# Performance work log

Measured on AMD Instinct MI355X. Metric: run time of the kernel, lower is better.

The kernel has to match this reference:

```python
import jax, jax.numpy as jnp
import numpy as np

B, N, C, H, L, M, V, NC = 8, 2048, 512, 8, 8, 128, 32000, 2
HD = C // H          # head dim = 64
HID = 4 * C          # MLP hidden = 2048
SCALE = HD ** -0.5
LN_EPS = 1e-5
FEAT_EPS = 1e-6


def _orth_matrix(d, m, rng):
    # gaussian_orthogonal_random_matrix: stack QR blocks of d x d
    blocks = []
    n_full, m_rem = divmod(m, d)
    for _ in range(n_full):
        Q, _ = np.linalg.qr(rng.standard_normal((d, d)))
        blocks.append(Q)
    if m_rem > 0:
        Q, _ = np.linalg.qr(rng.standard_normal((d, d)))
        blocks.append(Q[:, :m_rem])
    return np.concatenate(blocks, axis=1)


def setup_inputs() -> dict:
    key = jax.random.key(0)
    ks = jax.random.split(key, 32)
    rng = np.random.default_rng(0)

    def w(i, shape, s=0.02):
        return jax.random.normal(ks[i], shape, jnp.float32) * s

    proj = jnp.asarray(
        np.stack([np.stack([_orth_matrix(HD, M, rng) for _ in range(H)]) for _ in range(L)]),
        jnp.float32)  # [L, H, HD, M]

    inp = {
        "input_ids": jax.random.randint(ks[0], (B, N), 0, V),
        "attention_mask": jnp.ones((B, N), jnp.int32),
        "tok_emb": w(1, (V, C)),
        "cls": w(2, (1, 1, C)),
        "pos": w(3, (N + 1, C)),
        "ln1_g": jnp.ones((L, C), jnp.float32),
        "ln1_b": jnp.zeros((L, C), jnp.float32),
        "qW": w(4, (L, C, C)), "qb": jnp.zeros((L, C), jnp.float32),
        "kW": w(5, (L, C, C)), "kb": jnp.zeros((L, C), jnp.float32),
        "vW": w(6, (L, C, C)), "vb": jnp.zeros((L, C), jnp.float32),
        "oW": w(7, (L, C, C)), "ob": jnp.zeros((L, C), jnp.float32),
        "proj": proj,
        "ln2_g": jnp.ones((L, C), jnp.float32),
        "ln2_b": jnp.zeros((L, C), jnp.float32),
        "fc1W": w(8, (L, C, HID)), "fc1b": jnp.zeros((L, HID), jnp.float32),
        "fc2W": w(9, (L, HID, C)), "fc2b": jnp.zeros((L, C), jnp.float32),
        "lnf_g": jnp.ones((C,), jnp.float32),
        "lnf_b": jnp.zeros((C,), jnp.float32),
        "headW": w(10, (C, NC)),
        "headb": jnp.zeros((NC,), jnp.float32),
    }
    return inp


def _ln(x, g, b):
    mu = jnp.mean(x, axis=-1, keepdims=True)
    var = jnp.mean((x - mu) ** 2, axis=-1, keepdims=True)
    return (x - mu) * jax.lax.rsqrt(var + LN_EPS) * g + b


def _softmax_feature(x, p):
    # x: [B,Nt,H,HD], p: [H,HD,M]
    xw = jnp.einsum('bnhd,hdm->bnhm', x, p)
    x_sq = 0.5 * jnp.sum(x * x, axis=-1, keepdims=True)
    mx = jnp.max(xw, axis=-1, keepdims=True)
    return jnp.exp(xw - mx) * jnp.exp(mx - x_sq) + FEAT_EPS


def reference(input_ids, attention_mask, tok_emb, cls, pos, ln1_g, ln1_b,
              qW, qb, kW, kb, vW, vb, oW, ob, proj, ln2_g, ln2_b,
              fc1W, fc1b, fc2W, fc2b, lnf_g, lnf_b, headW, headb):
    x = tok_emb[input_ids]                                   # [B,N,C]
    x = jnp.concatenate([jnp.broadcast_to(cls, (B, 1, C)), x], axis=1)  # [B,Nt,C]
    x = x + pos[None]
    mask = jnp.concatenate(
        [jnp.ones((B, 1), x.dtype), attention_mask.astype(x.dtype)], axis=1)  # [B,Nt]
    mfeat = mask[:, :, None, None]

    Nt = N + 1
    for i in range(L):
        # Performer attention (FAVOR+)
        y = _ln(x, ln1_g[i], ln1_b[i])
        q = (y @ qW[i] + qb[i]).reshape(B, Nt, H, HD) * SCALE
        k = (y @ kW[i] + kb[i]).reshape(B, Nt, H, HD) * mfeat
        v = (y @ vW[i] + vb[i]).reshape(B, Nt, H, HD) * mfeat
        qf = _softmax_feature(q, proj[i])                    # [B,Nt,H,M]
        kf = _softmax_feature(k, proj[i])
        kv = jnp.einsum('bnhm,bnhd->bhmd', kf, v)            # [B,H,M,HD]
        ksum = jnp.sum(kf, axis=1)                           # [B,H,M]
        denom = jnp.maximum(jnp.einsum('bnhm,bhm->bhn', qf, ksum), 1e-6)[..., None]
        ctx = jnp.einsum('bnhm,bhmd->bhnd', qf, kv) / denom  # [B,H,Nt,HD]
        out = ctx.transpose(0, 2, 1, 3).reshape(B, Nt, C)
        x = x + (out @ oW[i] + ob[i])
        # MLP (exact GELU, as nn.GELU default)
        y = _ln(x, ln2_g[i], ln2_b[i])
        h = jax.nn.gelu(y @ fc1W[i] + fc1b[i], approximate=False)
        x = x + (h @ fc2W[i] + fc2b[i])

    x = _ln(x, lnf_g, lnf_b)
    return x[:, 0] @ headW + headb                           # [B,NC]
```

## Files before the change

### kernel.cpp

```cpp
#include <hip/hip_runtime.h>
#include <cmath>
#include <cstdint>
#include <cstddef>

#define B_ 8
#define N_ 2048
#define NT 2049
#define NP 2080
#define C_ 512
#define H_ 8
#define HD_ 64
#define L_ 8
#define M_ 128
#define HID_ 2048
#define NC_ 2
#define BNT (B_*NT)
#define RP (B_*NP)
#define SCALE_ 0.125f
#define LN_EPS_ 1e-5f
#define FEAT_EPS_ 1e-6f

#define MODE_GELU  2
#define MODE_RESID 3

typedef unsigned short u16;
typedef unsigned short u16x8 __attribute__((ext_vector_type(8)));
typedef short frag __attribute__((ext_vector_type(8)));
typedef float f32x4 __attribute__((ext_vector_type(4)));

constexpr size_t F_X    = 0;
constexpr size_t F_KVP  = F_X   + (size_t)RP*512;
constexpr size_t F_KSP  = F_KVP + (size_t)4*64*8192;
constexpr size_t F_KV   = F_KSP + (size_t)4*64*128;
constexpr size_t F_KS   = F_KV  + (size_t)64*M_*HD_;
constexpr size_t F_QKVB = F_KS  + (size_t)64*M_;
constexpr size_t F_END  = F_QKVB + 1536;
constexpr size_t S_BASE = 2 * F_END;
constexpr size_t S_Y    = S_BASE;
constexpr size_t S_V    = S_Y  + (size_t)RP*512;
constexpr size_t S_KF   = S_V  + (size_t)RP*512;
constexpr size_t S_QF   = S_KF + (size_t)RP*1024;
constexpr size_t S_WQKV = S_QF + (size_t)RP*1024;
constexpr size_t S_WO   = S_WQKV + (size_t)1536*512;
constexpr size_t S_WF1  = S_WO   + (size_t)512*512;
constexpr size_t S_WF2  = S_WF1  + (size_t)2048*512;
constexpr size_t S_PT   = S_WF2  + (size_t)512*2048;
constexpr size_t S_END  = S_PT   + (size_t)8*128*64;
constexpr size_t WS_BYTES = S_END * 2;

__device__ __forceinline__ float wave_reduce(float v) {
#pragma unroll
  for (int off = 32; off > 0; off >>= 1) v += __shfl_down(v, off, 64);
  return v;
}
__device__ __forceinline__ float b2f(u16 u) {
  union { float f; uint32_t i; } v; v.i = ((uint32_t)u) << 16; return v.f;
}
__device__ __forceinline__ u16 f2b(float f) {
  union { float f; uint32_t i; } v; v.f = f;
  uint32_t r = v.i + 0x7FFF + ((v.i >> 16) & 1);
  return (u16)(r >> 16);
}
__device__ __forceinline__ void gstage(const u16* g, u16* lds_base, int lane) {
#if __has_builtin(__builtin_amdgcn_global_load_lds)
  __builtin_amdgcn_global_load_lds((const __attribute__((address_space(1))) void*)g,
      (__attribute__((address_space(3))) void*)lds_base, 16, 0, 0);
#else
  *(u16x8*)(lds_base + lane * 8) = *(const u16x8*)g;
#endif
}

__global__ __launch_bounds__(256) void embed_k(const int* __restrict__ ids,
    const float* __restrict__ tok, const float* __restrict__ cls,
    const float* __restrict__ pos, float* __restrict__ X) {
  int row = blockIdx.x;
  int b = row / NT, n = row - b * NT;
  int t = threadIdx.x;
  const float* src = (n == 0) ? cls : tok + (size_t)ids[b * N_ + n - 1] * C_;
  size_t rp = (size_t)b * NP + n;
  X[rp * C_ + t]       = src[t]       + pos[(size_t)n * C_ + t];
  X[rp * C_ + t + 256] = src[t + 256] + pos[(size_t)n * C_ + t + 256];
}

__global__ __launch_bounds__(256) void wconv_k(
    const float* __restrict__ qW, const float* __restrict__ kW,
    const float* __restrict__ vW, const float* __restrict__ oW,
    const float* __restrict__ f1W, const float* __restrict__ f2W,
    const float* __restrict__ projL,
    const float* __restrict__ qb, const float* __restrict__ kb,
    const float* __restrict__ vb,
    u16* __restrict__ Wqkv, u16* __restrict__ Wo,
    u16* __restrict__ Wf1, u16* __restrict__ Wf2,
    u16* __restrict__ PT, float* __restrict__ QKVB) {
  __shared__ float tile[32][33];
  int bid = blockIdx.x, t = threadIdx.x;
  if (bid >= 3104) {
    int i = (bid - 3104) * 256 + t;
    QKVB[i] = (i < 512) ? qb[i] : (i < 1024) ? kb[i - 512] : vb[i - 1024];
    return;
  }
  if (bid >= 3072) {
    int base = (bid - 3072) * 2048 + t * 8;
#pragma unroll
    for (int j = 0; j < 8; ++j) {
      int idx = base + j;
      int h = idx >> 13, rem = idx & 8191, m = rem >> 6, d = rem & 63;
      PT[idx] = f2b(projL[(size_t)h * 8192 + d * 128 + m]);
    }
    return;
  }
  int ti = t >> 5, tj = t & 31;
  const float* src; u16* dst; int k0, n0, ldn, ldk, scol;
  if (bid < 768) {
    int tk = bid & 15, tn = bid >> 4;
    k0 = tk * 32; n0 = tn * 32;
    int sel = n0 >> 9; scol = n0 & 511;
    src = (sel == 0) ? qW : (sel == 1) ? kW : vW;
    ldn = 512; dst = Wqkv; ldk = 512;
  } else if (bid < 1024) {
    int b2 = bid - 768;
    int tk = b2 & 15, tn = b2 >> 4;
    k0 = tk * 32; n0 = tn * 32; scol = n0;
    src = oW; ldn = 512; dst = Wo; ldk = 512;
  } else if (bid < 2048) {
    int b2 = bid - 1024;
    int tk = b2 & 15, tn = b2 >> 4;
    k0 = tk * 32; n0 = tn * 32; scol = n0;
    src = f1W; ldn = 2048; dst = Wf1; ldk = 512;
  } else {
    int b2 = bid - 2048;
    int tk = b2 & 63, tn = b2 >> 6;
    k0 = tk * 32; n0 = tn * 32; scol = n0;
    src = f2W; ldn = 512; dst = Wf2; ldk = 2048;
  }
  const float* sp = src + (size_t)k0 * ldn + scol;
  u16* dp = dst + (size_t)n0 * ldk + k0;
#pragma unroll
  for (int p = 0; p < 4; ++p)
    tile[ti + p * 8][tj] = sp[(size_t)(ti + p * 8) * ldn + tj];
  __syncthreads();
#pragma unroll
  for (int p = 0; p < 4; ++p)
    dp[(size_t)(ti + p * 8) * ldk + tj] = f2b(tile[tj][ti + p * 8]);
}

__global__ __launch_bounds__(256) void ln_bf_k(const float* __restrict__ X,
    const float* __restrict__ g, const float* __restrict__ b,
    u16* __restrict__ Y) {
  int w = threadIdx.x >> 6, lane = threadIdx.x & 63;
  int row = blockIdx.x * 4 + w;
  const float* xr = X + (size_t)row * C_;
  float v[8];
  *(float4*)&v[0] = *(const float4*)(xr + lane * 8);
  *(float4*)&v[4] = *(const float4*)(xr + lane * 8 + 4);
  float s = 0.f;
#pragma unroll
  for (int j = 0; j < 8; ++j) s += v[j];
  s = wave_reduce(s);
  float mu = __shfl(s, 0, 64) * (1.0f / C_);
  float sq = 0.f;
#pragma unroll
  for (int j = 0; j < 8; ++j) { float d = v[j] - mu; sq = fmaf(d, d, sq); }
  sq = wave_reduce(sq);
  float rs = rsqrtf(__shfl(sq, 0, 64) * (1.0f / C_) + LN_EPS_);
  float gv[8], bv[8];
  *(float4*)&gv[0] = *(const float4*)(g + lane * 8);
  *(float4*)&gv[4] = *(const float4*)(g + lane * 8 + 4);
  *(float4*)&bv[0] = *(const float4*)(b + lane * 8);
  *(float4*)&bv[4] = *(const float4*)(b + lane * 8 + 4);
  u16x8 o;
#pragma unroll
  for (int j = 0; j < 8; ++j) o[j] = f2b((v[j] - mu) * rs * gv[j] + bv[j]);
  *(u16x8*)(Y + (size_t)row * C_ + lane * 8) = o;
}

__global__ __launch_bounds__(256) void gemm_bf_k(
    const u16* __restrict__ A, int lda,
    const u16* __restrict__ Wt,
    const float* __restrict__ bias,
    float* __restrict__ outF, u16* __restrict__ outB,
    int ldc, int Kdim, int mode) {
  __shared__ __align__(16) u16 As[128 * 64];
  __shared__ __align__(16) u16 Bs[128 * 64];
  const int t = threadIdx.x, w = t >> 6, l = t & 63;
  const int row0 = blockIdx.y * 128, col0 = blockIdx.x * 128;
  const int wm = w & 1, wn = w >> 1;
  const int lm = l & 15, lkb = l >> 4;
  const int lr = l >> 3, lc = l & 7;
  const int kch = (lc ^ lr) * 8;
  const u16* Ag = A  + (size_t)(row0 + lr) * lda  + kch;
  const u16* Bg = Wt + (size_t)(col0 + lr) * Kdim + kch;
  const int sx = lm & 7;
  f32x4 acc[4][4] = {};
  for (int k0 = 0; k0 < Kdim; k0 += 64) {
    __syncthreads();
#pragma unroll
    for (int j = 0; j < 4; ++j) {
      int c8 = w * 4 + j;
      gstage(Ag + (size_t)c8 * 8 * lda  + k0, &As[c8 * 512], l);
      gstage(Bg + (size_t)c8 * 8 * Kdim + k0, &Bs[c8 * 512], l);
    }
    __syncthreads();
#pragma unroll
    for (int ks = 0; ks < 2; ++ks) {
      frag af[4], bf4[4];
#pragma unroll
      for (int i = 0; i < 4; ++i)
        af[i] = *(const frag*)&As[(wm * 64 + i * 16 + lm) * 64 + (((ks * 4 + lkb) ^ sx) * 8)];
#pragma unroll
      for (int j = 0; j < 4; ++j)
        bf4[j] = *(const frag*)&Bs[(wn * 64 + j * 16 + lm) * 64 + (((ks * 4 + lkb) ^ sx) * 8)];
#pragma unroll
      for (int i = 0; i < 4; ++i)
#pragma unroll
        for (int j = 0; j < 4; ++j)
          acc[i][j] = __builtin_amdgcn_mfma_f32_16x16x32_bf16(af[i], bf4[j], acc[i][j], 0, 0, 0);
    }
  }
#pragma unroll
  for (int i = 0; i < 4; ++i) {
#pragma unroll
    for (int r = 0; r < 4; ++r) {
      int grow = row0 + wm * 64 + i * 16 + lkb * 4 + r;
      if (mode == MODE_RESID) {
        float* orow = outF + (size_t)grow * ldc + col0;
#pragma unroll
        for (int j = 0; j < 4; ++j) {
          int gc = wn * 64 + j * 16 + lm;
          orow[gc] += acc[i][j][r] + bias[col0 + gc];
        }
      } else {
        u16* orow = outB + (size_t)grow * ldc + col0;
#pragma unroll
        for (int j = 0; j < 4; ++j) {
          int gc = wn * 64 + j * 16 + lm;
          float v = acc[i][j][r] + bias[col0 + gc];
          float u = v * (1.5957691216f + 0.0713548162f * v * v);
          v = v / (1.f + __expf(-u));
          orow[gc] = f2b(v);
        }
      }
    }
  }
}

__global__ __launch_bounds__(256) void gemm_bf64_k(
    const u16* __restrict__ A, int lda,
    const u16* __restrict__ Wt,
    const float* __restrict__ bias,
    float* __restrict__ outF, u16* __restrict__ outB,
    int ldc, int Kdim, int mode) {
  __shared__ __align__(16) u16 As[64 * 64];
  __shared__ __align__(16) u16 Bs[128 * 64];
  const int t = threadIdx.x, w = t >> 6, l = t & 63;
  const int row0 = blockIdx.y * 64, col0 = blockIdx.x * 128;
  const int wm = w & 1, wn = w >> 1;
  const int lm = l & 15, lkb = l >> 4;
  const int lr = l >> 3, lc = l & 7;
  const int kch = (lc ^ lr) * 8;
  const u16* Ag = A  + (size_t)(row0 + lr) * lda  + kch;
  const u16* Bg = Wt + (size_t)(col0 + lr) * Kdim + kch;
  const int sx = lm & 7;
  f32x4 acc[2][4] = {};
  for (int k0 = 0; k0 < Kdim; k0 += 64) {
    __syncthreads();
#pragma unroll
    for (int q = 0; q < 2; ++q) {
      int c8 = w * 2 + q;
      gstage(Ag + (size_t)c8 * 8 * lda + k0, &As[c8 * 512], l);
    }
#pragma unroll
    for (int q = 0; q < 4; ++q) {
      int c8 = w * 4 + q;
      gstage(Bg + (size_t)c8 * 8 * Kdim + k0, &Bs[c8 * 512], l);
    }
    __syncthreads();
#pragma unroll
    for (int ks = 0; ks < 2; ++ks) {
      frag af[2], bf4[4];
#pragma unroll
      for (int i = 0; i < 2; ++i)
        af[i] = *(const frag*)&As[(wm * 32 + i * 16 + lm) * 64 + (((ks * 4 + lkb) ^ sx) * 8)];
#pragma unroll
      for (int j = 0; j < 4; ++j)
        bf4[j] = *(const frag*)&Bs[(wn * 64 + j * 16 + lm) * 64 + (((ks * 4 + lkb) ^ sx) * 8)];
#pragma unroll
      for (int i = 0; i < 2; ++i)
#pragma unroll
        for (int j = 0; j < 4; ++j)
          acc[i][j] = __builtin_amdgcn_mfma_f32_16x16x32_bf16(af[i], bf4[j], acc[i][j], 0, 0, 0);
    }
  }
#pragma unroll
  for (int i = 0; i < 2; ++i) {
#pragma unroll
    for (int r = 0; r < 4; ++r) {
      int grow = row0 + wm * 32 + i * 16 + lkb * 4 + r;
      if (mode == MODE_RESID) {
        float* orow = outF + (size_t)grow * ldc + col0;
#pragma unroll
        for (int j = 0; j < 4; ++j) {
          int gc = wn * 64 + j * 16 + lm;
          orow[gc] += acc[i][j][r] + bias[col0 + gc];
        }
      } else {
        u16* orow = outB + (size_t)grow * ldc + col0;
#pragma unroll
        for (int j = 0; j < 4; ++j) {
          int gc = wn * 64 + j * 16 + lm;
          float v = acc[i][j][r] + bias[col0 + gc];
          float u = v * (1.5957691216f + 0.0713548162f * v * v);
          v = v / (1.f + __expf(-u));
          orow[gc] = f2b(v);
        }
      }
    }
  }
}

__global__ __launch_bounds__(256) void gemmqkv_k(
    const u16* __restrict__ A,
    const u16* __restrict__ Wt,
    const float* __restrict__ bias,
    u16* __restrict__ Vout,
    u16* __restrict__ QF, u16* __restrict__ KF,
    const u16* __restrict__ PT,
    const int* __restrict__ attn) {
  __shared__ __align__(16) u16 As[128 * 64];
  __shared__ __align__(16) u16 Bs[128 * 64];
  __shared__ __align__(16) u16 ptb[128 * 64];
  __shared__ float sxe[128][2];
  const int t = threadIdx.x, w = t >> 6, l = t & 63;
  const int cx = blockIdx.x;
  const int row0 = blockIdx.y * 128, col0 = cx * 128;
  const int wm = w & 1, wn = w >> 1;
  const int lm = l & 15, lkb = l >> 4;
  const int lr = l >> 3, lc = l & 7;
  const int kch = (lc ^ lr) * 8;
  const u16* Ag = A  + (size_t)(row0 + lr) * 512 + kch;
  const u16* Bg = Wt + (size_t)(col0 + lr) * 512 + kch;
  const int sx = lm & 7;
  f32x4 acc[4][4] = {};
  for (int k0 = 0; k0 < 512; k0 += 64) {
    __syncthreads();
#pragma unroll
    for (int j = 0; j < 4; ++j) {
      int c8 = w * 4 + j;
      gstage(Ag + (size_t)c8 * 8 * 512 + k0, &As[c8 * 512], l);
      gstage(Bg + (size_t)c8 * 8 * 512 + k0, &Bs[c8 * 512], l);
    }
    __syncthreads();
#pragma unroll
    for (int ks = 0; ks < 2; ++ks) {
      frag af[4], bf4[4];
#pragma unroll
      for (int i = 0; i < 4; ++i)
        af[i] = *(const frag*)&As[(wm * 64 + i * 16 + lm) * 64 + (((ks * 4 + lkb) ^ sx) * 8)];
#pragma unroll
      for (int j = 0; j < 4; ++j)
        bf4[j] = *(const frag*)&Bs[(wn * 64 + j * 16 + lm) * 64 + (((ks * 4 + lkb) ^ sx) * 8)];
#pragma unroll
      for (int i = 0; i < 4; ++i)
#pragma unroll
        for (int j = 0; j < 4; ++j)
          acc[i][j] = __builtin_amdgcn_mfma_f32_16x16x32_bf16(af[i], bf4[j], acc[i][j], 0, 0, 0);
    }
  }
  if (cx >= 8) {
    int c0v = col0 - 1024;
#pragma unroll
    for (int i = 0; i < 4; ++i) {
#pragma unroll
      for (int r = 0; r < 4; ++r) {
        int grow = row0 + wm * 64 + i * 16 + lkb * 4 + r;
        int bb = grow / NP, nn = grow - bb * NP;
        float mrow = (nn == 0) ? 1.f : ((nn < NT) ? (float)attn[bb * N_ + nn - 1] : 0.f);
        u16* orow = Vout + (size_t)grow * 512 + c0v;
#pragma unroll
        for (int j = 0; j < 4; ++j) {
          int gc = wn * 64 + j * 16 + lm;
          orow[gc] = f2b((acc[i][j][r] + bias[col0 + gc]) * mrow);
        }
      }
    }
    return;
  }
  const bool isq = (cx < 4);
  const int hbase = (isq ? cx : cx - 4) * 2;
  __syncthreads();
  {
    u16* qt = wn ? Bs : As;
#pragma unroll
    for (int i = 0; i < 4; ++i) {
#pragma unroll
      for (int r = 0; r < 4; ++r) {
        int rl = wm * 64 + i * 16 + lkb * 4 + r;
        float mrow;
        if (isq) mrow = SCALE_;
        else {
          int grow = row0 + rl;
          int bb = grow / NP, nn = grow - bb * NP;
          mrow = (nn == 0) ? 1.f : ((nn < NT) ? (float)attn[bb * N_ + nn - 1] : 0.f);
        }
#pragma unroll
        for (int j = 0; j < 4; ++j) {
          int gcc = j * 16 + lm;
          float v = (acc[i][j][r] + bias[col0 + wn * 64 + gcc]) * mrow;
          qt[rl * 64 + (((gcc >> 3) ^ (rl & 7)) * 8) + (gcc & 7)] = f2b(v);
        }
      }
    }
  }
  {
    const u16* Pg = PT + (size_t)hbase * 8192 + (size_t)lr * 64 + kch;
#pragma unroll
    for (int q = 0; q < 4; ++q) {
      int c8 = w * 4 + q;
      gstage(Pg + (size_t)c8 * 8 * 64, &ptb[c8 * 512], l);
    }
  }
  __syncthreads();
  {
    int rowi = t >> 1, hf = t & 1;
    const u16* qq = hf ? Bs : As;
    float s = 0.f;
#pragma unroll
    for (int c = 0; c < 8; ++c) {
      const u16* p = &qq[rowi * 64 + ((c ^ (rowi & 7)) * 8)];
#pragma unroll
      for (int e = 0; e < 8; ++e) { float a = b2f(p[e]); s = fmaf(a, a, s); }
    }
    sxe[rowi][hf] = 0.5f * s;
  }
  __syncthreads();
  u16* OF = isq ? QF : KF;
#pragma unroll
  for (int hp = 0; hp < 2; ++hp) {
    if (hp == 1) {
      __syncthreads();
      const u16* Pg = PT + (size_t)(hbase + 1) * 8192 + (size_t)lr * 64 + kch;
#pragma unroll
      for (int q = 0; q < 4; ++q) {
        int c8 = w * 4 + q;
        gstage(Pg + (size_t)c8 * 8 * 64, &ptb[c8 * 512], l);
      }
      __syncthreads();
    }
    const u16* qt = hp ? Bs : As;
    f32x4 a2[2][8] = {};
#pragma unroll
    for (int ks = 0; ks < 2; ++ks) {
      frag af2[2], bf2[8];
#pragma unroll
      for (int i = 0; i < 2; ++i)
        af2[i] = *(const frag*)&qt[(w * 32 + i * 16 + lm) * 64 + (((ks * 4 + lkb) ^ sx) * 8)];
#pragma unroll
      for (int j = 0; j < 8; ++j)
        bf2[j] = *(const frag*)&ptb[(j * 16 + lm) * 64 + (((ks * 4 + lkb) ^ sx) * 8)];
#pragma unroll
      for (int i = 0; i < 2; ++i)
#pragma unroll
        for (int j = 0; j < 8; ++j)
          a2[i][j] = __builtin_amdgcn_mfma_f32_16x16x32_bf16(af2[i], bf2[j], a2[i][j], 0, 0, 0);
    }
    int hg = hbase + hp;
#pragma unroll
    for (int i = 0; i < 2; ++i) {
#pragma unroll
      for (int r = 0; r < 4; ++r) {
        int R = w * 32 + i * 16 + lkb * 4 + r;
        int grow = row0 + R;
        int bb = grow / NP, nn = grow - bb * NP;
        bool valid = nn < NT;
        float xs = sxe[R][hp];
        u16* orow = OF + (size_t)grow * 1024 + (size_t)hg * 128;
#pragma unroll
        for (int j = 0; j < 8; ++j) {
          int m = j * 16 + lm;
          float v = valid ? (__expf(a2[i][j][r] - xs) + FEAT_EPS_) : 0.f;
          orow[m] = f2b(v);
        }
      }
    }
  }
}

__global__ __launch_bounds__(256) void kvpart_k(const u16* __restrict__ KF,
    const u16* __restrict__ Vb, float* __restrict__ KVP,
    float* __restrict__ KSP) {
  int ci = blockIdx.x, bh = blockIdx.y;
  int b = bh >> 3, h = bh & 7;
  size_t rb0 = (size_t)b * NP + ci * 520;
  __shared__ __align__(16) float kfs[8 * 132];
  __shared__ __align__(16) float vsm[8 * 68];
  int t = threadIdx.x;
  const int d0 = (t & 7) * 8, m0 = (t >> 3) * 4;
  float acc[4][8] = {};
  float ks[4] = {};
  for (int tile = 0; tile < 65; ++tile) {
    size_t rb = rb0 + tile * 8;
#pragma unroll
    for (int p = 0; p < 4; ++p) {
      int e = p * 256 + t; int m = e & 127; int tok = e >> 7;
      kfs[tok * 132 + m] = b2f(KF[(rb + tok) * 1024 + h * 128 + m]);
    }
#pragma unroll
    for (int p = 0; p < 2; ++p) {
      int e = p * 256 + t; int d = e & 63; int tok = e >> 6;
      vsm[tok * 68 + d] = b2f(Vb[(rb + tok) * 512 + h * 64 + d]);
    }
    __syncthreads();
#pragma unroll
    for (int tok = 0; tok < 8; ++tok) {
      float kq[4], va[8];
      *(float4*)&kq[0] = *(const float4*)&kfs[tok * 132 + m0];
      *(float4*)&va[0] = *(const float4*)&vsm[tok * 68 + d0];
      *(float4*)&va[4] = *(const float4*)&vsm[tok * 68 + d0 + 4];
#pragma unroll
      for (int mi = 0; mi < 4; ++mi)
#pragma unroll
        for (int di = 0; di < 8; ++di)
          acc[mi][di] = fmaf(kq[mi], va[di], acc[mi][di]);
      if ((t & 7) == 0) { ks[0] += kq[0]; ks[1] += kq[1]; ks[2] += kq[2]; ks[3] += kq[3]; }
    }
    __syncthreads();
  }
  size_t base = ((size_t)ci * 64 + bh) * 8192;
#pragma unroll
  for (int mi = 0; mi < 4; ++mi)
#pragma unroll
    for (int di = 0; di < 8; ++di)
      KVP[base + (size_t)(m0 + mi) * 64 + d0 + di] = acc[mi][di];
  if ((t & 7) == 0) {
#pragma unroll
    for (int mi = 0; mi < 4; ++mi)
      KSP[((size_t)ci * 64 + bh) * 128 + m0 + mi] = ks[mi];
  }
}

__global__ __launch_bounds__(256) void kvred_k(const float* __restrict__ KVP,
    const float* __restrict__ KSP, float* __restrict__ KV,
    float* __restrict__ KSUM) {
  int bh = blockIdx.x, t = threadIdx.x;
#pragma unroll
  for (int p = 0; p < 32; ++p) {
    int e = p * 256 + t;
    float s = 0.f;
#pragma unroll
    for (int ci = 0; ci < 4; ++ci) s += KVP[((size_t)ci * 64 + bh) * 8192 + e];
    KV[(size_t)bh * 8192 + e] = s;
  }
  if (t < 128) {
    float s = 0.f;
#pragma unroll
    for (int ci = 0; ci < 4; ++ci) s += KSP[((size_t)ci * 64 + bh) * 128 + t];
    KSUM[(size_t)bh * 128 + t] = s;
  }
}

__global__ __launch_bounds__(256) void ctx_k(const u16* __restrict__ QF,
    const float* __restrict__ KVg, const float* __restrict__ KSUM,
    u16* __restrict__ CTXo) {
  __shared__ float qfs[128 * 36];
  __shared__ float kvs[128 * 68];
  __shared__ float ksums[128];
  __shared__ float dls[32];
  __shared__ float dpart[8 * 32];
  int t = threadIdx.x;
  int bh = blockIdx.y; int b = bh >> 3, h = bh & 7;
  int n0 = blockIdx.x * 32;
  size_t rbase = (size_t)b * NP + n0;
#pragma unroll
  for (int p = 0; p < 16; ++p) {
    int e = p * 256 + t; int m = e & 127; int tok = e >> 7;
    qfs[m * 36 + tok] = b2f(QF[(rbase + tok) * 1024 + h * 128 + m]);
  }
#pragma unroll
  for (int p = 0; p < 32; ++p) {
    int e = p * 256 + t;
    kvs[(e >> 6) * 68 + (e & 63)] = KVg[(size_t)bh * 8192 + e];
  }
  if (t < 128) ksums[t] = KSUM[bh * 128 + t];
  __syncthreads();
  {
    int j = t & 31, pp = t >> 5;
    float s = 0.f;
#pragma unroll
    for (int mi = 0; mi < 16; ++mi) {
      int m = pp * 16 + mi;
      s = fmaf(qfs[m * 36 + j], ksums[m], s);
    }
    dpart[pp * 32 + j] = s;
  }
  __syncthreads();
  if (t < 32) {
    float den = 0.f;
#pragma unroll
    for (int pp = 0; pp < 8; ++pp) den += dpart[pp * 32 + t];
    dls[t] = 1.f / fmaxf(den, 1e-6f);
  }
  __syncthreads();
  {
    const int d0 = (t & 15) * 4, tok0 = (t >> 4) * 2;
    float acc[2][4] = {};
#pragma unroll 16
    for (int m = 0; m < 128; ++m) {
      float q0 = qfs[m * 36 + tok0];
      float q1 = qfs[m * 36 + tok0 + 1];
      float4 kv4 = *(const float4*)&kvs[m * 68 + d0];
      acc[0][0] = fmaf(q0, kv4.x, acc[0][0]); acc[0][1] = fmaf(q0, kv4.y, acc[0][1]);
      acc[0][2] = fmaf(q0, kv4.z, acc[0][2]); acc[0][3] = fmaf(q0, kv4.w, acc[0][3]);
      acc[1][0] = fmaf(q1, kv4.x, acc[1][0]); acc[1][1] = fmaf(q1, kv4.y, acc[1][1]);
      acc[1][2] = fmaf(q1, kv4.z, acc[1][2]); acc[1][3] = fmaf(q1, kv4.w, acc[1][3]);
    }
#pragma unroll
    for (int r = 0; r < 2; ++r) {
      int n = n0 + tok0 + r;
      if (n >= NT) continue;
      float rd = dls[tok0 + r];
      u16* o = CTXo + (rbase + tok0 + r) * C_ + h * HD_ + d0;
#pragma unroll
      for (int c = 0; c < 4; ++c) o[c] = f2b(acc[r][c] * rd);
    }
  }
}

__global__ __launch_bounds__(256) void final_k(const float* __restrict__ X,
    const float* __restrict__ g, const float* __restrict__ beta,
    const float* __restrict__ hW, const float* __restrict__ hb,
    float* __restrict__ out) {
  int b = blockIdx.x, t = threadIdx.x;
  const float* xr = X + (size_t)b * NP * C_;
  float v0 = xr[t], v1 = xr[t + 256];
  __shared__ float red[4][4];
  float s = wave_reduce(v0 + v1);
  if ((t & 63) == 0) red[0][t >> 6] = s;
  __syncthreads();
  float mu = (red[0][0] + red[0][1] + red[0][2] + red[0][3]) * (1.0f / C_);
  float d0 = v0 - mu, d1 = v1 - mu;
  float s2 = wave_reduce(d0 * d0 + d1 * d1);
  if ((t & 63) == 0) red[1][t >> 6] = s2;
  __syncthreads();
  float var = (red[1][0] + red[1][1] + red[1][2] + red[1][3]) * (1.0f / C_);
  float rs = rsqrtf(var + LN_EPS_);
  float n0 = d0 * rs * g[t] + beta[t];
  float n1 = d1 * rs * g[t + 256] + beta[t + 256];
  float p0 = n0 * hW[t * NC_]     + n1 * hW[(t + 256) * NC_];
  float p1 = n0 * hW[t * NC_ + 1] + n1 * hW[(t + 256) * NC_ + 1];
  float t0 = wave_reduce(p0);
  float t1 = wave_reduce(p1);
  if ((t & 63) == 0) { red[2][t >> 6] = t0; red[3][t >> 6] = t1; }
  __syncthreads();
  if (t == 0) {
    out[b * NC_]     = red[2][0] + red[2][1] + red[2][2] + red[2][3] + hb[0];
    out[b * NC_ + 1] = red[3][0] + red[3][1] + red[3][2] + red[3][3] + hb[1];
  }
}

extern "C" void kernel_launch(void* const* d_in, const int* in_sizes, int n_in,
                              void* d_out, int out_size, void* d_ws, size_t ws_size,
                              hipStream_t stream) {
  if (ws_size < WS_BYTES) return;
  const int*   ids   = (const int*)d_in[0];
  const int*   attn  = (const int*)d_in[1];
  const float* tok   = (const float*)d_in[2];
  const float* cls   = (const float*)d_in[3];
  const float* pos   = (const float*)d_in[4];
  const float* ln1g  = (const float*)d_in[5];
  const float* ln1b  = (const float*)d_in[6];
  const float* qW    = (const float*)d_in[7];
  const float* qb    = (const float*)d_in[8];
  const float* kW    = (const float*)d_in[9];
  const float* kb    = (const float*)d_in[10];
  const float* vW    = (const float*)d_in[11];
  const float* vb    = (const float*)d_in[12];
  const float* oW    = (const float*)d_in[13];
  const float* ob    = (const float*)d_in[14];
  const float* proj  = (const float*)d_in[15];
  const float* ln2g  = (const float*)d_in[16];
  const float* ln2b  = (const float*)d_in[17];
  const float* fc1W  = (const float*)d_in[18];
  const float* fc1b  = (const float*)d_in[19];
  const float* fc2W  = (const float*)d_in[20];
  const float* fc2b  = (const float*)d_in[21];
  const float* lnfg  = (const float*)d_in[22];
  const float* lnfb  = (const float*)d_in[23];
  const float* headW = (const float*)d_in[24];
  const float* headb = (const float*)d_in[25];

  float* ws  = (float*)d_ws;
  u16*   wsu = (u16*)d_ws;
  float* X    = ws + F_X;
  float* KVP  = ws + F_KVP;
  float* KSP  = ws + F_KSP;
  float* KV   = ws + F_KV;
  float* KSUM = ws + F_KS;
  float* QKVB = ws + F_QKVB;
  u16* Ybf  = wsu + S_Y;
  u16* CTXb = wsu + S_Y;
  u16* Vb   = wsu + S_V;
  u16* HB   = wsu + S_V;
  u16* KFb  = wsu + S_KF;
  u16* QFb  = wsu + S_QF;
  u16* Wqkv = wsu + S_WQKV;
  u16* Wo   = wsu + S_WO;
  u16* Wf1  = wsu + S_WF1;
  u16* Wf2  = wsu + S_WF2;
  u16* PT   = wsu + S_PT;

  embed_k<<<BNT, 256, 0, stream>>>(ids, tok, cls, pos, X);
  for (int i = 0; i < L_; ++i) {
    wconv_k<<<3110, 256, 0, stream>>>(qW + (size_t)i * C_ * C_, kW + (size_t)i * C_ * C_,
        vW + (size_t)i * C_ * C_, oW + (size_t)i * C_ * C_,
        fc1W + (size_t)i * C_ * HID_, fc2W + (size_t)i * HID_ * C_,
        proj + (size_t)i * H_ * HD_ * M_,
        qb + i * C_, kb + i * C_, vb + i * C_,
        Wqkv, Wo, Wf1, Wf2, PT, QKVB);
    ln_bf_k<<<RP / 4, 256, 0, stream>>>(X, ln1g + i * C_, ln1b + i * C_, Ybf);
    gemmqkv_k<<<dim3(12, 130), 256, 0, stream>>>(Ybf, Wqkv, QKVB,
        Vb, QFb, KFb, PT, attn);
    kvpart_k<<<dim3(4, 64), 256, 0, stream>>>(KFb, Vb, KVP, KSP);
    kvred_k<<<64, 256, 0, stream>>>(KVP, KSP, KV, KSUM);
    ctx_k<<<dim3(65, 64), 256, 0, stream>>>(QFb, KV, KSUM, CTXb);
    gemm_bf64_k<<<dim3(4, 260), 256, 0, stream>>>(CTXb, 512, Wo, ob + i * C_,
        X, nullptr, 512, 512, MODE_RESID);
    ln_bf_k<<<RP / 4, 256, 0, stream>>>(X, ln2g + i * C_, ln2b + i * C_, Ybf);
    gemm_bf_k<<<dim3(16, 130), 256, 0, stream>>>(Ybf, 512, Wf1,
        fc1b + i * HID_, nullptr, HB, 2048, 512, MODE_GELU);
    gemm_bf64_k<<<dim3(4, 260), 256, 0, stream>>>(HB, 2048, Wf2,
        fc2b + i * C_, X, nullptr, 512, 2048, MODE_RESID);
  }
  final_k<<<B_, 256, 0, stream>>>(X, lnfg, lnfb, headW, headb, (float*)d_out);
}
```

Before: 3.444 ms.

## Add XCD-aware block swizzle to GEMMs and prefetch KV tiles in registers

Adds a block-index remap that groups consecutive logical tiles onto the same XCD, so neighbouring tiles that share A/B panels hit the same L2. It is applied to the GEMM, QKV-feature and ctx kernels. Separately, kvpart_k now loads K-feature and V tiles with 16-byte vector loads into registers and prefetches the next tile during compute instead of using scalar bf16 loads. This gives better cache locality and overlaps global latency, at the cost of some extra registers and index math.

```diff
diff --git a/kernel.cpp b/kernel.cpp
--- a/kernel.cpp
+++ b/kernel.cpp
@@ -68,6 +68,15 @@
 #else
   *(u16x8*)(lds_base + lane * 8) = *(const u16x8*)g;
 #endif
+}
+__device__ __forceinline__ void xcd_swz(int& bx, int& by) {
+  int gx = gridDim.x;
+  int nwg = gx * gridDim.y;
+  int hw = blockIdx.x + blockIdx.y * gx;
+  if (nwg & 7) { bx = blockIdx.x; by = blockIdx.y; return; }
+  int cpx = nwg >> 3;
+  int swz = (hw & 7) * cpx + (hw >> 3);
+  bx = swz % gx; by = swz / gx;
 }
 
 __global__ __launch_bounds__(256) void embed_k(const int* __restrict__ ids,
@@ -183,7 +192,8 @@
   __shared__ __align__(16) u16 As[128 * 64];
   __shared__ __align__(16) u16 Bs[128 * 64];
   const int t = threadIdx.x, w = t >> 6, l = t & 63;
-  const int row0 = blockIdx.y * 128, col0 = blockIdx.x * 128;
+  int bx, by; xcd_swz(bx, by);
+  const int row0 = by * 128, col0 = bx * 128;
   const int wm = w & 1, wn = w >> 1;
   const int lm = l & 15, lkb = l >> 4;
   const int lr = l >> 3, lc = l & 7;
@@ -253,7 +263,8 @@
   __shared__ __align__(16) u16 As[64 * 64];
   __shared__ __align__(16) u16 Bs[128 * 64];
   const int t = threadIdx.x, w = t >> 6, l = t & 63;
-  const int row0 = blockIdx.y * 64, col0 = blockIdx.x * 128;
+  int bx, by; xcd_swz(bx, by);
+  const int row0 = by * 64, col0 = bx * 128;
   const int wm = w & 1, wn = w >> 1;
   const int lm = l & 15, lkb = l >> 4;
   const int lr = l >> 3, lc = l & 7;
@@ -331,8 +342,9 @@
   __shared__ __align__(16) u16 ptb[128 * 64];
   __shared__ float sxe[128][2];
   const int t = threadIdx.x, w = t >> 6, l = t & 63;
-  const int cx = blockIdx.x;
-  const int row0 = blockIdx.y * 128, col0 = cx * 128;
+  int bx, by; xcd_swz(bx, by);
+  const int cx = bx;
+  const int row0 = by * 128, col0 = cx * 128;
   const int wm = w & 1, wn = w >> 1;
   const int lm = l & 15, lkb = l >> 4;
   const int lr = l >> 3, lc = l & 7;
@@ -495,21 +507,30 @@
   __shared__ __align__(16) float vsm[8 * 68];
   int t = threadIdx.x;
   const int d0 = (t & 7) * 8, m0 = (t >> 3) * 4;
+  const bool hk = t < 128;
+  const bool hv = (t >= 128) && (t < 192);
+  const int ktok = t >> 4, kmj = (t & 15) * 8;
+  const int vtok = (t - 128) >> 3, vdj = (t & 7) * 8;
   float acc[4][8] = {};
   float ks[4] = {};
+  u16x8 rk, rv;
+  if (hk) rk = *(const u16x8*)&KF[(rb0 + ktok) * 1024 + h * 128 + kmj];
+  if (hv) rv = *(const u16x8*)&Vb[(rb0 + vtok) * 512 + h * 64 + vdj];
   for (int tile = 0; tile < 65; ++tile) {
-    size_t rb = rb0 + tile * 8;
-#pragma unroll
-    for (int p = 0; p < 4; ++p) {
-      int e = p * 256 + t; int m = e & 127; int tok = e >> 7;
-      kfs[tok * 132 + m] = b2f(KF[(rb + tok) * 1024 + h * 128 + m]);
-    }
-#pragma unroll
-    for (int p = 0; p < 2; ++p) {
-      int e = p * 256 + t; int d = e & 63; int tok = e >> 6;
-      vsm[tok * 68 + d] = b2f(Vb[(rb + tok) * 512 + h * 64 + d]);
+    if (hk) {
+#pragma unroll
+      for (int e = 0; e < 8; ++e) kfs[ktok * 132 + kmj + e] = b2f(rk[e]);
+    }
+    if (hv) {
+#pragma unroll
+      for (int e = 0; e < 8; ++e) vsm[vtok * 68 + vdj + e] = b2f(rv[e]);
     }
     __syncthreads();
+    if (tile + 1 < 65) {
+      size_t rb = rb0 + (size_t)(tile + 1) * 8;
+      if (hk) rk = *(const u16x8*)&KF[(rb + ktok) * 1024 + h * 128 + kmj];
+      if (hv) rv = *(const u16x8*)&Vb[(rb + vtok) * 512 + h * 64 + vdj];
+    }
 #pragma unroll
     for (int tok = 0; tok < 8; ++tok) {
       float kq[4], va[8];
@@ -567,8 +588,9 @@
   __shared__ float dls[32];
   __shared__ float dpart[8 * 32];
   int t = threadIdx.x;
-  int bh = blockIdx.y; int b = bh >> 3, h = bh & 7;
-  int n0 = blockIdx.x * 32;
+  int bx, by; xcd_swz(bx, by);
+  int bh = by; int b = bh >> 3, h = bh & 7;
+  int n0 = bx * 32;
   size_t rbase = (size_t)b * NP + n0;
 #pragma unroll
   for (int p = 0; p < 16; ++p) {
```

Measured after the change: 3.193 ms. 1.08x faster.
